# Kernel optimization log

Hardware: AMD Instinct MI355X
Metric: run time of the kernel (lower is better)

## Reference

```python
import jax, jax.numpy as jnp
import numpy as np

B, M, D, H, DH = 4, 2048, 1024, 16, 64
R_ATTN, FFN_D, R_FFN = 32, 4096, 512
ROPE_THETA = 10000.0
LN_EPS = 1e-5


def layernorm(x, w, b):
    mu = jnp.mean(x, axis=-1, keepdims=True)
    var = jnp.mean(jnp.square(x - mu), axis=-1, keepdims=True)
    return (x - mu) * jax.lax.rsqrt(var + LN_EPS) * w + b


def headwise_svd(x, U, V, b):
    # x: [B,M,D]; U: [H,D,r]; V: [H,r,dh] -> [B,M,H,dh]
    xr = jnp.einsum('bmd,hdr->bmhr', x, U)
    y = jnp.einsum('bmhr,hrk->bmhk', xr, V)
    return y + b.reshape(U.shape[0], -1)


def rotate_half(x):
    x1, x2 = jnp.split(x, 2, axis=-1)
    return jnp.concatenate([-x2, x1], axis=-1)


def rope_cos_sin(m, dh, dtype):
    inv_freq = 1.0 / (ROPE_THETA ** (jnp.arange(0, dh, 2, dtype=jnp.float32) / dh))
    freqs = jnp.arange(m, dtype=jnp.float32)[:, None] * inv_freq[None, :]  # [M, dh/2]
    emb = jnp.concatenate([freqs, freqs], axis=-1)  # [M, dh]
    return jnp.cos(emb).astype(dtype), jnp.sin(emb).astype(dtype)


def setup_inputs() -> dict:
    key = jax.random.key(0)
    ks = jax.random.split(key, 16)
    s = 0.02
    def n(k, shape, scale=s):
        return jax.random.normal(k, shape, dtype=jnp.float32) * scale
    return dict(
        hidden_states=jax.random.normal(ks[0], (B, M, D), dtype=jnp.float32),
        attention_mask=jnp.ones((B, M), dtype=jnp.int32),
        ln1_w=jnp.ones((D,), jnp.float32), ln1_b=jnp.zeros((D,), jnp.float32),
        Uq=n(ks[1], (H, D, R_ATTN)), Vq=n(ks[2], (H, R_ATTN, DH)), bq=jnp.zeros((D,), jnp.float32),
        Uk=n(ks[3], (H, D, R_ATTN)), Vk=n(ks[4], (H, R_ATTN, DH)), bk=jnp.zeros((D,), jnp.float32),
        Uv=n(ks[5], (H, D, R_ATTN)), Vv=n(ks[6], (H, R_ATTN, DH)), bv=jnp.zeros((D,), jnp.float32),
        Wo_attn=n(ks[7], (D, D)), bo_attn=jnp.zeros((D,), jnp.float32),
        ln2_w=jnp.ones((D,), jnp.float32), ln2_b=jnp.zeros((D,), jnp.float32),
        U_wi=n(ks[8], (D, R_FFN)), V_wi=n(ks[9], (R_FFN, 2 * FFN_D)), b_wi=jnp.zeros((2 * FFN_D,), jnp.float32),
        U_wo=n(ks[10], (FFN_D, R_FFN)), V_wo=n(ks[11], (R_FFN, D)), b_wo=jnp.zeros((D,), jnp.float32),
    )


def reference(hidden_states, attention_mask, ln1_w, ln1_b,
              Uq, Vq, bq, Uk, Vk, bk, Uv, Vv, bv,
              Wo_attn, bo_attn, ln2_w, ln2_b,
              U_wi, V_wi, b_wi, U_wo, V_wo, b_wo):
    x = hidden_states
    xn = layernorm(x, ln1_w, ln1_b)

    # head-wise low-rank SVD QKV projections -> [B,H,M,dh]
    q = headwise_svd(xn, Uq, Vq, bq).transpose(0, 2, 1, 3)
    k = headwise_svd(xn, Uk, Vk, bk).transpose(0, 2, 1, 3)
    v = headwise_svd(xn, Uv, Vv, bv).transpose(0, 2, 1, 3)

    cos, sin = rope_cos_sin(x.shape[1], q.shape[-1], q.dtype)  # [M, dh], broadcasts
    q = q * cos + rotate_half(q) * sin
    k = k * cos + rotate_half(k) * sin

    scale = 1.0 / jnp.sqrt(jnp.asarray(q.shape[-1], q.dtype))
    scores = jnp.einsum('bhqd,bhkd->bhqk', q, k) * scale
    pad = (attention_mask == 0)[:, None, None, :]  # [B,1,1,M]
    scores = jnp.where(pad, jnp.finfo(scores.dtype).min, scores)
    attn = jax.nn.softmax(scores, axis=-1)
    ctx = jnp.einsum('bhqk,bhkd->bhqd', attn, v)
    ctx = ctx.transpose(0, 2, 1, 3).reshape(x.shape)  # [B,M,D]
    attn_out = jnp.einsum('bmd,ed->bme', ctx, Wo_attn) + bo_attn  # dense Wo (torch Linear)
    x = x + attn_out

    # FFN: low-rank Wi -> GEGLU(tanh) -> low-rank Wo
    xn2 = layernorm(x, ln2_w, ln2_b)
    h = (xn2 @ U_wi) @ V_wi + b_wi  # [B,M,2*FFN_D]
    h1, h2 = jnp.split(h, 2, axis=-1)
    g = jax.nn.gelu(h1, approximate=True) * h2  # GEGLU, tanh approx
    ffn_out = (g @ U_wo) @ V_wo + b_wo
    return x + ffn_out
```

## Files before the change

### kernel.cpp

```cpp
#include <hip/hip_runtime.h>
#include <cstdint>

#define DEV __device__ __forceinline__

typedef __attribute__((ext_vector_type(8))) short bf16x8;
typedef __attribute__((ext_vector_type(4))) float f32x4;
typedef __attribute__((ext_vector_type(16))) float f32x16;

#define MFMA(a,b,c) __builtin_amdgcn_mfma_f32_16x16x32_bf16((a),(b),(c),0,0,0)
#define MFMA32(a,b,c) __builtin_amdgcn_mfma_f32_32x32x16_bf16((a),(b),(c),0,0,0)

DEV unsigned short f2bf(float f) {
  union { float f; unsigned u; } v; v.f = f;
  unsigned r = v.u + 0x7fffu + ((v.u >> 16) & 1u);
  return (unsigned short)(r >> 16);
}
DEV float bf2f(unsigned short s) {
  union { unsigned u; float f; } v; v.u = ((unsigned)s) << 16; return v.f;
}
DEV float max3f(float a, float b, float c) { return fmaxf(fmaxf(a, b), c); }

DEV void gload16(const unsigned short* g, short* l) {
  __builtin_amdgcn_global_load_lds(
      (const __attribute__((address_space(1))) unsigned*)g,
      (__attribute__((address_space(3))) unsigned*)l, 16, 0, 0);
}


__global__ void k_build_ut(const float* __restrict__ Uq, const float* __restrict__ Uk,
                           const float* __restrict__ Uv, unsigned short* __restrict__ Ut) {
  __shared__ float tile[32][33];
  int s = blockIdx.y;
  int proj = s >> 4, h = s & 15;
  const float* U = (proj == 0) ? Uq : (proj == 1) ? Uk : Uv;
  const float* Us = U + (size_t)h * 1024 * 32;
  int d0 = blockIdx.x * 32;
  int tx = threadIdx.x, ty = threadIdx.y;
#pragma unroll
  for (int i = ty; i < 32; i += 8)
    tile[i][tx] = Us[(size_t)(d0 + i) * 32 + tx];
  __syncthreads();
#pragma unroll
  for (int i = ty; i < 32; i += 8)
    Ut[(size_t)(s * 32 + i) * 1024 + d0 + tx] = f2bf(tile[tx][i]);
}

__global__ void k_build_vt(const float* __restrict__ Vq, const float* __restrict__ Vk,
                           const float* __restrict__ Vv, unsigned short* __restrict__ Vt) {
  int ph = blockIdx.x;
  int proj = ph >> 4, h = ph & 15;
  const float* V = (proj == 0) ? Vq : (proj == 1) ? Vk : Vv;
  const float* Vs = V + (size_t)h * 2048;
  int t = threadIdx.x;
#pragma unroll
  for (int idx = t; idx < 2048; idx += 256) {
    int dh = idx >> 5, r = idx & 31;
    Vt[(size_t)ph * 2048 + idx] = f2bf(Vs[r * 64 + dh]);
  }
}

__global__ void k_f2bf(const float* __restrict__ in, unsigned short* __restrict__ out, int n) {
  int i = blockIdx.x * 256 + threadIdx.x;
  if (i < n) out[i] = f2bf(in[i]);
}

__global__ void k_transpose_bf16(const float* __restrict__ in, unsigned short* __restrict__ out,
                                 int R, int C) {
  __shared__ float tile[32][33];
  int c0 = blockIdx.x * 32, r0 = blockIdx.y * 32;
  int tx = threadIdx.x, ty = threadIdx.y;
#pragma unroll
  for (int i = ty; i < 32; i += 8)
    tile[i][tx] = in[(size_t)(r0 + i) * C + c0 + tx];
  __syncthreads();
#pragma unroll
  for (int i = ty; i < 32; i += 8)
    out[(size_t)(c0 + i) * R + r0 + tx] = f2bf(tile[tx][i]);
}

__global__ __launch_bounds__(256) void k_layernorm(const float* __restrict__ x,
                                                   const float* __restrict__ w,
                                                   const float* __restrict__ b,
                                                   unsigned short* __restrict__ out) {
  int lane = threadIdx.x & 63, wid = threadIdx.x >> 6;
  size_t row = (size_t)blockIdx.x * 4 + wid;
  const float4* xr = (const float4*)(x + row * 1024);
  float4 v[4];
  float s = 0.f, s2 = 0.f;
#pragma unroll
  for (int t = 0; t < 4; ++t) {
    v[t] = xr[lane + t * 64];
    s += v[t].x + v[t].y + v[t].z + v[t].w;
    s2 += v[t].x * v[t].x + v[t].y * v[t].y + v[t].z * v[t].z + v[t].w * v[t].w;
  }
#pragma unroll
  for (int o = 1; o < 64; o <<= 1) { s += __shfl_xor(s, o); s2 += __shfl_xor(s2, o); }
  float mean = s * (1.f / 1024.f);
  float var = s2 * (1.f / 1024.f) - mean * mean;
  float inv = rsqrtf(var + 1e-5f);
  unsigned long long* op = (unsigned long long*)(out + row * 1024);
#pragma unroll
  for (int t = 0; t < 4; ++t) {
    float4 wv = ((const float4*)w)[lane + t * 64];
    float4 bv = ((const float4*)b)[lane + t * 64];
    union { unsigned short u[4]; unsigned long long ll; } o;
    o.u[0] = f2bf((v[t].x - mean) * inv * wv.x + bv.x);
    o.u[1] = f2bf((v[t].y - mean) * inv * wv.y + bv.y);
    o.u[2] = f2bf((v[t].z - mean) * inv * wv.z + bv.z);
    o.u[3] = f2bf((v[t].w - mean) * inv * wv.w + bv.w);
    op[lane + t * 64] = o.ll;
  }
}

template <int EPI>
__global__ __launch_bounds__(256, 4) void k_gemm(const unsigned short* __restrict__ A,
                                                 const unsigned short* __restrict__ Bt,
                                                 const float* __restrict__ bias,
                                                 const float* __restrict__ resid,
                                                 void* __restrict__ outp, int N, int K) {
  __shared__ short Al[128 * 32];
  __shared__ short Bl[128 * 32];
  int tid = threadIdx.x, lane = tid & 63, wid = tid >> 6;
  int wr = wid >> 1, wc = wid & 1;
  size_t row0 = (size_t)blockIdx.y * 128;
  int col0 = blockIdx.x * 128;
  int arow = lane >> 2, acol = (lane & 3) << 3;
  const unsigned short* Ag = A + (row0 + wid * 32 + arow) * K + acol;
  const unsigned short* Bg = Bt + ((size_t)(col0 + wid * 32 + arow)) * K + acol;
  short* Ald = Al + wid * 1024;
  short* Bld = Bl + wid * 1024;
  f32x4 acc[4][4] = {};
  int fr = lane & 15, fk = (lane >> 4) << 3;
  for (int k0 = 0; k0 < K; k0 += 32) {
    __syncthreads();
    gload16(Ag + k0, Ald);
    gload16(Ag + (size_t)16 * K + k0, Ald + 512);
    gload16(Bg + k0, Bld);
    gload16(Bg + (size_t)16 * K + k0, Bld + 512);
    __syncthreads();
    bf16x8 af[4], bfr[4];
#pragma unroll
    for (int i = 0; i < 4; ++i) {
      af[i] = *(const bf16x8*)&Al[(wr * 64 + i * 16 + fr) * 32 + fk];
      bfr[i] = *(const bf16x8*)&Bl[(wc * 64 + i * 16 + fr) * 32 + fk];
    }
#pragma unroll
    for (int i = 0; i < 4; ++i)
#pragma unroll
      for (int j = 0; j < 4; ++j) acc[i][j] = MFMA(af[i], bfr[j], acc[i][j]);
  }
  int cr = (lane >> 4) << 2, cc = lane & 15;
#pragma unroll
  for (int j = 0; j < 4; ++j) {
    int col = col0 + wc * 64 + j * 16 + cc;
    float bb = (EPI >= 1) ? bias[col] : 0.f;
#pragma unroll
    for (int i = 0; i < 4; ++i) {
#pragma unroll
      for (int r = 0; r < 4; ++r) {
        size_t row = row0 + wr * 64 + i * 16 + cr + r;
        float v = acc[i][j][r] + bb;
        if (EPI == 2)
          ((float*)outp)[row * N + col] = v + resid[row * N + col];
        else
          ((unsigned short*)outp)[row * N + col] = f2bf(v);
      }
    }
  }
}

__global__ __launch_bounds__(256, 4) void k_gemm64(const unsigned short* __restrict__ A,
                                                   const unsigned short* __restrict__ Bt,
                                                   unsigned short* __restrict__ out,
                                                   int N, int K) {
  __shared__ short Al[128 * 32];
  __shared__ short Bl[64 * 32];
  int tid = threadIdx.x, lane = tid & 63, wid = tid >> 6;
  size_t row0 = (size_t)blockIdx.y * 128;
  int col0 = blockIdx.x * 64;
  int arow = lane >> 2, acol = (lane & 3) << 3;
  const unsigned short* Ag = A + (row0 + wid * 32 + arow) * K + acol;
  const unsigned short* Bg = Bt + ((size_t)(col0 + wid * 16 + arow)) * K + acol;
  short* Ald = Al + wid * 1024;
  short* Bld = Bl + wid * 512;
  f32x4 acc[2][4] = {};
  int fr = lane & 15, fk = (lane >> 4) << 3;
  for (int k0 = 0; k0 < K; k0 += 32) {
    __syncthreads();
    gload16(Ag + k0, Ald);
    gload16(Ag + (size_t)16 * K + k0, Ald + 512);
    gload16(Bg + k0, Bld);
    __syncthreads();
    bf16x8 af[2], bfr[4];
#pragma unroll
    for (int i = 0; i < 2; ++i)
      af[i] = *(const bf16x8*)&Al[(wid * 32 + i * 16 + fr) * 32 + fk];
#pragma unroll
    for (int j = 0; j < 4; ++j)
      bfr[j] = *(const bf16x8*)&Bl[(j * 16 + fr) * 32 + fk];
#pragma unroll
    for (int i = 0; i < 2; ++i)
#pragma unroll
      for (int j = 0; j < 4; ++j) acc[i][j] = MFMA(af[i], bfr[j], acc[i][j]);
  }
  int cr = (lane >> 4) << 2, cc = lane & 15;
#pragma unroll
  for (int j = 0; j < 4; ++j) {
    int col = col0 + j * 16 + cc;
#pragma unroll
    for (int i = 0; i < 2; ++i) {
#pragma unroll
      for (int r = 0; r < 4; ++r) {
        size_t row = row0 + wid * 32 + i * 16 + cr + r;
        out[row * N + col] = f2bf(acc[i][j][r]);
      }
    }
  }
}

__global__ __launch_bounds__(256, 2) void k_qkv(const unsigned short* __restrict__ A,
                                                const unsigned short* __restrict__ Ut,
                                                const unsigned short* __restrict__ Vt,
                                                const float* __restrict__ bq,
                                                const float* __restrict__ bk,
                                                const float* __restrict__ bv,
                                                unsigned short* __restrict__ qkv,
                                                unsigned short* __restrict__ vT) {
  __shared__ short Al[128 * 32];
  __shared__ short Bl[128 * 32];
  __shared__ short Xr[4][64 * 72];
  const int K = 1024, N3 = 3072;
  int tid = threadIdx.x, lane = tid & 63, wid = tid >> 6;
  int wr = wid >> 1, wc = wid & 1;
  size_t row0 = (size_t)blockIdx.y * 128;
  int col0 = blockIdx.x * 128;
  int arow = lane >> 2, acol = (lane & 3) << 3;
  const unsigned short* Ag = A + (row0 + wid * 32 + arow) * K + acol;
  const unsigned short* Bg = Ut + ((size_t)(col0 + wid * 32 + arow)) * K + acol;
  short* Ald = Al + wid * 1024;
  short* Bld = Bl + wid * 1024;
  f32x4 acc[4][4] = {};
  int fr = lane & 15, fk = (lane >> 4) << 3;
  for (int k0 = 0; k0 < K; k0 += 32) {
    __syncthreads();
    gload16(Ag + k0, Ald);
    gload16(Ag + (size_t)16 * K + k0, Ald + 512);
    gload16(Bg + k0, Bld);
    gload16(Bg + (size_t)16 * K + k0, Bld + 512);
    __syncthreads();
    bf16x8 af[4], bfr[4];
#pragma unroll
    for (int i = 0; i < 4; ++i) {
      af[i] = *(const bf16x8*)&Al[(wr * 64 + i * 16 + fr) * 32 + fk];
      bfr[i] = *(const bf16x8*)&Bl[(wc * 64 + i * 16 + fr) * 32 + fk];
    }
#pragma unroll
    for (int i = 0; i < 4; ++i)
#pragma unroll
      for (int j = 0; j < 4; ++j) acc[i][j] = MFMA(af[i], bfr[j], acc[i][j]);
  }
  int cr = (lane >> 4) << 2, cc = lane & 15;
  short* xw = &Xr[wid][0];
#pragma unroll
  for (int j = 0; j < 4; ++j)
#pragma unroll
    for (int i = 0; i < 4; ++i)
#pragma unroll
      for (int r = 0; r < 4; ++r)
        xw[(i * 16 + cr + r) * 72 + j * 16 + cc] = (short)f2bf(acc[i][j][r]);
  int phbase = blockIdx.x * 4 + wc * 2;
  const f32x4 zero4 = {0.f, 0.f, 0.f, 0.f};
#pragma unroll
  for (int h2 = 0; h2 < 2; ++h2) {
    int ph = phbase + h2;
    int proj = ph >> 4, hh = ph & 15;
    bf16x8 af2[4], bf2[4];
#pragma unroll
    for (int i2 = 0; i2 < 4; ++i2)
      af2[i2] = *(const bf16x8*)&xw[(i2 * 16 + fr) * 72 + h2 * 32 + fk];
#pragma unroll
    for (int j2 = 0; j2 < 4; ++j2)
      bf2[j2] = *(const bf16x8*)(Vt + ((size_t)ph * 64 + j2 * 16 + fr) * 32 + fk);
    f32x4 a2[4][4];
#pragma unroll
    for (int i2 = 0; i2 < 4; ++i2)
#pragma unroll
      for (int j2 = 0; j2 < 4; ++j2) a2[i2][j2] = MFMA(af2[i2], bf2[j2], zero4);
    const float* bp = (proj == 0) ? bq : (proj == 1) ? bk : bv;
    if (proj == 2) {
      int bq_ = (int)(row0 >> 11);
      int tok0 = (int)(row0 & 2047) + wr * 64;
      unsigned short* vtb = vT + ((size_t)(bq_ * 16 + hh) * 64) * 2048;
#pragma unroll
      for (int j2 = 0; j2 < 4; ++j2) {
        int dh = j2 * 16 + cc;
        float bb = bp[hh * 64 + dh];
        unsigned short* vrow = vtb + (size_t)dh * 2048;
#pragma unroll
        for (int i2 = 0; i2 < 4; ++i2) {
          union { unsigned short u[4]; unsigned long long ll; } o;
#pragma unroll
          for (int r = 0; r < 4; ++r) o.u[r] = f2bf(a2[i2][j2][r] + bb);
          *(unsigned long long*)(vrow + tok0 + i2 * 16 + cr) = o.ll;
        }
      }
    } else {
      int obase = proj * 1024 + hh * 64;
      float sc = (proj == 0) ? 0.18033688011112042f : 1.f;
#pragma unroll
      for (int j2 = 0; j2 < 2; ++j2) {
        int irot = j2 * 16 + cc;
        float freq = __expf((float)irot * -0.28782313662425575f);
        float bb1 = bp[hh * 64 + irot];
        float bb2 = bp[hh * 64 + irot + 32];
#pragma unroll
        for (int i2 = 0; i2 < 4; ++i2)
#pragma unroll
          for (int r = 0; r < 4; ++r) {
            size_t row = row0 + wr * 64 + i2 * 16 + cr + r;
            int m = (int)(row & 2047);
            float x1v = a2[i2][j2][r] + bb1;
            float x2v = a2[i2][j2 + 2][r] + bb2;
            float sn, csn;
            __sincosf((float)m * freq, &sn, &csn);
            qkv[row * N3 + obase + irot] = f2bf((x1v * csn - x2v * sn) * sc);
            qkv[row * N3 + obase + irot + 32] = f2bf((x2v * csn + x1v * sn) * sc);
          }
      }
    }
  }
}

__global__ __launch_bounds__(256, 2) void k_gemm_geglu(const unsigned short* __restrict__ A,
                                                       const unsigned short* __restrict__ Bt,
                                                       const float* __restrict__ bias,
                                                       unsigned short* __restrict__ out) {
  __shared__ short Al[128 * 32];
  __shared__ short B1l[128 * 32];
  __shared__ short B2l[128 * 32];
  const int K = 512;
  int tid = threadIdx.x, lane = tid & 63, wid = tid >> 6;
  int wr = wid >> 1, wc = wid & 1;
  size_t row0 = (size_t)blockIdx.y * 128;
  int col0 = blockIdx.x * 128;
  int arow = lane >> 2, acol = (lane & 3) << 3;
  const unsigned short* Ag = A + (row0 + wid * 32 + arow) * K + acol;
  const unsigned short* B1g = Bt + ((size_t)(col0 + wid * 32 + arow)) * K + acol;
  const unsigned short* B2g = Bt + ((size_t)(col0 + 4096 + wid * 32 + arow)) * K + acol;
  short* Ald = Al + wid * 1024;
  short* B1d = B1l + wid * 1024;
  short* B2d = B2l + wid * 1024;
  f32x4 acc1[4][4] = {}, acc2[4][4] = {};
  int fr = lane & 15, fk = (lane >> 4) << 3;
  for (int k0 = 0; k0 < K; k0 += 32) {
    __syncthreads();
    gload16(Ag + k0, Ald);
    gload16(Ag + (size_t)16 * K + k0, Ald + 512);
    gload16(B1g + k0, B1d);
    gload16(B1g + (size_t)16 * K + k0, B1d + 512);
    gload16(B2g + k0, B2d);
    gload16(B2g + (size_t)16 * K + k0, B2d + 512);
    __syncthreads();
    bf16x8 af[4], b1f[4], b2f[4];
#pragma unroll
    for (int i = 0; i < 4; ++i) {
      af[i] = *(const bf16x8*)&Al[(wr * 64 + i * 16 + fr) * 32 + fk];
      b1f[i] = *(const bf16x8*)&B1l[(wc * 64 + i * 16 + fr) * 32 + fk];
      b2f[i] = *(const bf16x8*)&B2l[(wc * 64 + i * 16 + fr) * 32 + fk];
    }
#pragma unroll
    for (int i = 0; i < 4; ++i)
#pragma unroll
      for (int j = 0; j < 4; ++j) {
        acc1[i][j] = MFMA(af[i], b1f[j], acc1[i][j]);
        acc2[i][j] = MFMA(af[i], b2f[j], acc2[i][j]);
      }
  }
  int cr = (lane >> 4) << 2, cc = lane & 15;
#pragma unroll
  for (int j = 0; j < 4; ++j) {
    int col = col0 + wc * 64 + j * 16 + cc;
    float bb1 = bias[col], bb2 = bias[col + 4096];
#pragma unroll
    for (int i = 0; i < 4; ++i) {
#pragma unroll
      for (int r = 0; r < 4; ++r) {
        size_t row = row0 + wr * 64 + i * 16 + cr + r;
        float h1 = acc1[i][j][r] + bb1;
        float h2 = acc2[i][j][r] + bb2;
        float u = 0.7978845608028654f * (h1 + 0.044715f * h1 * h1 * h1);
        float e = __expf(2.f * u);
        float th = 1.f - 2.f / (e + 1.f);
        float gv = 0.5f * h1 * (1.f + th) * h2;
        out[row * 4096 + col] = f2bf(gv);
      }
    }
  }
}

#define KIX(r, c) ((r) * 64 + ((c) ^ (((r) & 7) << 3)))

__global__ __launch_bounds__(256, 4) void k_attn(const unsigned short* __restrict__ qkv,
                                                 const unsigned short* __restrict__ vT,
                                                 const int* __restrict__ mask,
                                                 unsigned short* __restrict__ ctx) {
  __shared__ short Kl[64 * 64];
  __shared__ short Vl[64 * 64];
  __shared__ short Ol[4][32 * 64];
  __shared__ float mpen[64];
  __shared__ int mflag;
  int bh = blockIdx.y, b = bh >> 4, h = bh & 15;
  int q0 = blockIdx.x << 7;
  int tid = threadIdx.x, lane = tid & 63, wid = tid >> 6;
  int qi = lane & 31, hi = lane >> 5;
  const unsigned short* qrow =
      qkv + ((size_t)(b * 2048 + q0 + wid * 32 + qi)) * 3072 + h * 64 + hi * 8;
  bf16x8 qa[4];
#pragma unroll
  for (int c = 0; c < 4; ++c) qa[c] = *(const bf16x8*)(qrow + c * 16);
  float m_r = -1e30f, l_r = 0.f;
  f32x16 oacc0 = {}, oacc1 = {};
  int srw = lane >> 3;
  int schx = ((lane & 7) ^ srw) << 3;
  int rb = wid * 16;
  const unsigned short* kgb =
      qkv + ((size_t)(b * 2048 + rb + srw)) * 3072 + 1024 + h * 64 + schx;
  const unsigned short* vgb = vT + ((size_t)(bh * 64 + rb + srw)) * 2048 + schx;
  short* kld = Kl + rb * 64;
  short* vld = Vl + rb * 64;
  const int* mbase = mask + b * 2048;
  const f32x16 zero16 = {};
  int mv = (tid < 64) ? mbase[tid] : 1;
  for (int k0 = 0; k0 < 2048; k0 += 64) {
    __syncthreads();
    gload16(kgb + (size_t)k0 * 3072, kld);
    gload16(kgb + (size_t)(k0 + 8) * 3072, kld + 512);
    gload16(vgb + k0, vld);
    gload16(vgb + (size_t)8 * 2048 + k0, vld + 512);
    if (wid == 0) {
      mpen[lane] = (mv == 0) ? -1e30f : 0.f;
      unsigned long long bal = __ballot(mv == 0);
      if (lane == 0) mflag = (bal != 0ull) ? 1 : 0;
    }
    if (k0 + 64 < 2048) mv = (tid < 64) ? mbase[k0 + 64 + tid] : 1;
    __syncthreads();
#pragma unroll
    for (int kt = 0; kt < 2; ++kt) {
      f32x16 s = zero16;
      __builtin_amdgcn_s_setprio(1);
#pragma unroll
      for (int c = 0; c < 4; ++c) {
        bf16x8 kf = *(const bf16x8*)&Kl[KIX(kt * 32 + qi, c * 16 + hi * 8)];
        s = MFMA32(kf, qa[c], s);
      }
      __builtin_amdgcn_s_setprio(0);
      if (mflag) {
        const f32x4* mp4 = (const f32x4*)mpen;
#pragma unroll
        for (int t = 0; t < 4; ++t) {
          f32x4 pen = mp4[kt * 8 + t * 2 + hi];
#pragma unroll
          for (int r = 0; r < 4; ++r) s[t * 4 + r] += pen[r];
        }
      }
      float t0 = max3f(s[0], s[1], s[2]);
      float t1 = max3f(s[3], s[4], s[5]);
      float t2 = max3f(s[6], s[7], s[8]);
      float t3 = max3f(s[9], s[10], s[11]);
      float t4 = max3f(s[12], s[13], s[14]);
      float t5 = fmaxf(t0, s[15]);
      float pmax = max3f(max3f(t5, t1, t2), t3, t4);
      pmax = fmaxf(pmax, __shfl_xor(pmax, 32));
      if (!__all(pmax - m_r <= 8.f)) {
        float mn = fmaxf(m_r, pmax);
        float fac = exp2f(m_r - mn);
        m_r = mn;
        l_r *= fac;
#pragma unroll
        for (int r = 0; r < 16; ++r) { oacc0[r] *= fac; oacc1[r] *= fac; }
      }
#pragma unroll
      for (int r = 0; r < 16; ++r) s[r] = exp2f(s[r] - m_r);
      float su0 = (s[0] + s[1]) + (s[2] + s[3]);
      float su1 = (s[4] + s[5]) + (s[6] + s[7]);
      float su2 = (s[8] + s[9]) + (s[10] + s[11]);
      float su3 = (s[12] + s[13]) + (s[14] + s[15]);
      l_r += (su0 + su1) + (su2 + su3);
      unsigned pk[8];
#pragma unroll
      for (int w = 0; w < 8; ++w)
        asm("v_cvt_pk_bf16_f32 %0, %1, %2" : "=v"(pk[w]) : "v"(s[2 * w]), "v"(s[2 * w + 1]));
      unsigned a0 = pk[0], b0 = pk[2];
      unsigned a1 = pk[1], b1 = pk[3];
      unsigned a2 = pk[4], b2 = pk[6];
      unsigned a3 = pk[5], b3 = pk[7];
      asm("v_permlane32_swap_b32 %0, %1" : "+v"(a0), "+v"(b0));
      asm("v_permlane32_swap_b32 %0, %1" : "+v"(a1), "+v"(b1));
      asm("v_permlane32_swap_b32 %0, %1" : "+v"(a2), "+v"(b2));
      asm("v_permlane32_swap_b32 %0, %1" : "+v"(a3), "+v"(b3));
      union { unsigned u[4]; bf16x8 v; } pb0, pb1;
      pb0.u[0] = a0; pb0.u[1] = a1; pb0.u[2] = b0; pb0.u[3] = b1;
      pb1.u[0] = a2; pb1.u[1] = a3; pb1.u[2] = b2; pb1.u[3] = b3;
      __builtin_amdgcn_s_setprio(1);
      {
        bf16x8 vf00 = *(const bf16x8*)&Vl[KIX(qi, kt * 32 + hi * 8)];
        bf16x8 vf01 = *(const bf16x8*)&Vl[KIX(qi, kt * 32 + 16 + hi * 8)];
        oacc0 = MFMA32(vf00, pb0.v, oacc0);
        oacc0 = MFMA32(vf01, pb1.v, oacc0);
        bf16x8 vf10 = *(const bf16x8*)&Vl[KIX(32 + qi, kt * 32 + hi * 8)];
        bf16x8 vf11 = *(const bf16x8*)&Vl[KIX(32 + qi, kt * 32 + 16 + hi * 8)];
        oacc1 = MFMA32(vf10, pb0.v, oacc1);
        oacc1 = MFMA32(vf11, pb1.v, oacc1);
      }
      __builtin_amdgcn_s_setprio(0);
    }
  }
  l_r += __shfl_xor(l_r, 32);
  float invl = 1.f / l_r;
  short* ob = &Ol[wid][0];
  int xsw = (qi & 7) << 3;
#pragma unroll
  for (int t = 0; t < 4; ++t) {
    int d = t * 8 + 4 * hi;
    float a0 = oacc0[4 * t] * invl, a1 = oacc0[4 * t + 1] * invl;
    float a2 = oacc0[4 * t + 2] * invl, a3 = oacc0[4 * t + 3] * invl;
    unsigned w0, w1;
    asm("v_cvt_pk_bf16_f32 %0, %1, %2" : "=v"(w0) : "v"(a0), "v"(a1));
    asm("v_cvt_pk_bf16_f32 %0, %1, %2" : "=v"(w1) : "v"(a2), "v"(a3));
    *(unsigned long long*)&ob[qi * 64 + (d ^ xsw)] =
        ((unsigned long long)w1 << 32) | (unsigned long long)w0;
    float c0 = oacc1[4 * t] * invl, c1 = oacc1[4 * t + 1] * invl;
    float c2 = oacc1[4 * t + 2] * invl, c3 = oacc1[4 * t + 3] * invl;
    unsigned w2, w3;
    asm("v_cvt_pk_bf16_f32 %0, %1, %2" : "=v"(w2) : "v"(c0), "v"(c1));
    asm("v_cvt_pk_bf16_f32 %0, %1, %2" : "=v"(w3) : "v"(c2), "v"(c3));
    *(unsigned long long*)&ob[qi * 64 + ((d + 32) ^ xsw)] =
        ((unsigned long long)w3 << 32) | (unsigned long long)w2;
  }
  __syncthreads();
#pragma unroll
  for (int p = 0; p < 2; ++p) {
    int q = p * 16 + (lane >> 2);
    int qx = (q & 7) << 3;
    unsigned short* dst =
        ctx + ((size_t)(b * 2048 + q0 + wid * 32 + q)) * 1024 + h * 64;
#pragma unroll
    for (int j = 0; j < 2; ++j) {
      int c = (lane & 3) * 8 + j * 32;
      bf16x8 vv = *(const bf16x8*)&ob[q * 64 + (c ^ qx)];
      __builtin_nontemporal_store(vv, (bf16x8*)(dst + c));
    }
  }
}

extern "C" void kernel_launch(void* const* d_in, const int* in_sizes, int n_in, void* d_out,
                              int out_size, void* d_ws, size_t ws_size, hipStream_t stream) {
  const float* x = (const float*)d_in[0];
  const int* amask = (const int*)d_in[1];
  const float* ln1w = (const float*)d_in[2];
  const float* ln1b = (const float*)d_in[3];
  const float* Uq = (const float*)d_in[4];
  const float* Vq = (const float*)d_in[5];
  const float* bq = (const float*)d_in[6];
  const float* Uk = (const float*)d_in[7];
  const float* Vk = (const float*)d_in[8];
  const float* bk = (const float*)d_in[9];
  const float* Uv = (const float*)d_in[10];
  const float* Vv = (const float*)d_in[11];
  const float* bv = (const float*)d_in[12];
  const float* Wo = (const float*)d_in[13];
  const float* bo = (const float*)d_in[14];
  const float* ln2w = (const float*)d_in[15];
  const float* ln2b = (const float*)d_in[16];
  const float* Uwi = (const float*)d_in[17];
  const float* Vwi = (const float*)d_in[18];
  const float* bwi = (const float*)d_in[19];
  const float* Uwo = (const float*)d_in[20];
  const float* Vwo = (const float*)d_in[21];
  const float* bwo = (const float*)d_in[22];

  char* ws = (char*)d_ws;
  size_t off = 0;
  auto alloc = [&](size_t bytes) {
    void* p = ws + off;
    off += (bytes + 255) & ~(size_t)255;
    return p;
  };
  unsigned short* xn = (unsigned short*)alloc((size_t)8192 * 1024 * 2);
  unsigned short* Ut = (unsigned short*)alloc((size_t)1536 * 1024 * 2);
  unsigned short* Vt = (unsigned short*)alloc((size_t)48 * 2048 * 2);
  unsigned short* Wob = (unsigned short*)alloc((size_t)1024 * 1024 * 2);
  unsigned short* Uwit = (unsigned short*)alloc((size_t)512 * 1024 * 2);
  unsigned short* Vwit = (unsigned short*)alloc((size_t)8192 * 512 * 2);
  unsigned short* Uwot = (unsigned short*)alloc((size_t)512 * 4096 * 2);
  unsigned short* Vwot = (unsigned short*)alloc((size_t)1024 * 512 * 2);
  unsigned short* qkv = (unsigned short*)alloc((size_t)8192 * 3072 * 2);
  unsigned short* ctx = (unsigned short*)alloc((size_t)8192 * 1024 * 2);
  float* x1 = (float*)alloc((size_t)8192 * 1024 * 4);
  unsigned short* hr = (unsigned short*)alloc((size_t)8192 * 512 * 2);
  unsigned short* gr = (unsigned short*)alloc((size_t)8192 * 512 * 2);
  unsigned short* g = qkv;
  unsigned short* xn2 = xn;
  unsigned short* vT = (unsigned short*)x1;
  if (off > ws_size) return;
  (void)in_sizes; (void)n_in; (void)out_size;

  dim3 tb(32, 8);
  k_build_ut<<<dim3(32, 48), tb, 0, stream>>>(Uq, Uk, Uv, Ut);
  k_build_vt<<<48, 256, 0, stream>>>(Vq, Vk, Vv, Vt);
  k_f2bf<<<4096, 256, 0, stream>>>(Wo, Wob, 1024 * 1024);
  k_transpose_bf16<<<dim3(512 / 32, 1024 / 32), tb, 0, stream>>>(Uwi, Uwit, 1024, 512);
  k_transpose_bf16<<<dim3(8192 / 32, 512 / 32), tb, 0, stream>>>(Vwi, Vwit, 512, 8192);
  k_transpose_bf16<<<dim3(512 / 32, 4096 / 32), tb, 0, stream>>>(Uwo, Uwot, 4096, 512);
  k_transpose_bf16<<<dim3(1024 / 32, 512 / 32), tb, 0, stream>>>(Vwo, Vwot, 512, 1024);

  k_layernorm<<<2048, 256, 0, stream>>>(x, ln1w, ln1b, xn);
  k_qkv<<<dim3(12, 64), 256, 0, stream>>>(xn, Ut, Vt, bq, bk, bv, qkv, vT);
  k_attn<<<dim3(16, 64), 256, 0, stream>>>(qkv, vT, amask, ctx);
  k_gemm<2><<<dim3(8, 64), 256, 0, stream>>>(ctx, Wob, bo, x, x1, 1024, 1024);
  k_layernorm<<<2048, 256, 0, stream>>>(x1, ln2w, ln2b, xn2);
  k_gemm64<<<dim3(8, 64), 256, 0, stream>>>(xn2, Uwit, hr, 512, 1024);
  k_gemm_geglu<<<dim3(32, 64), 256, 0, stream>>>(hr, Vwit, bwi, g);
  k_gemm64<<<dim3(8, 64), 256, 0, stream>>>(g, Uwot, gr, 512, 4096);
  k_gemm<2><<<dim3(8, 64), 256, 0, stream>>>(gr, Vwot, bwo, x1, d_out, 1024, 512);
}
```

Before: 474.1 us.

## Double-buffer K/V tiles in attention and precompute mask bits

The attention kernel now puts K and V into a two-stage shared-memory pool. The next 64-key tile is prefetched into the alternate buffer while the current one is computed, which drops one barrier per iteration. The per-tile mask penalty staging in shared memory is replaced by a ballot-built 32-bit mask computed up front, with per-element global reads only when a tile is masked. Shared memory per block grows to 32 KB, which could affect how many blocks fit per CU. Correctness depends on the top-of-loop barrier also waiting for the earlier async LDS loads to finish.

```diff
diff --git a/kernel.cpp b/kernel.cpp
--- a/kernel.cpp
+++ b/kernel.cpp
@@ -404,11 +404,7 @@
                                                  const unsigned short* __restrict__ vT,
                                                  const int* __restrict__ mask,
                                                  unsigned short* __restrict__ ctx) {
-  __shared__ short Kl[64 * 64];
-  __shared__ short Vl[64 * 64];
-  __shared__ short Ol[4][32 * 64];
-  __shared__ float mpen[64];
-  __shared__ int mflag;
+  __shared__ short pool[16384];
   int bh = blockIdx.y, b = bh >> 4, h = bh & 15;
   int q0 = blockIdx.x << 7;
   int tid = threadIdx.x, lane = tid & 63, wid = tid >> 6;
@@ -426,24 +422,35 @@
   const unsigned short* kgb =
       qkv + ((size_t)(b * 2048 + rb + srw)) * 3072 + 1024 + h * 64 + schx;
   const unsigned short* vgb = vT + ((size_t)(bh * 64 + rb + srw)) * 2048 + schx;
-  short* kld = Kl + rb * 64;
-  short* vld = Vl + rb * 64;
   const int* mbase = mask + b * 2048;
   const f32x16 zero16 = {};
-  int mv = (tid < 64) ? mbase[tid] : 1;
+  unsigned mbits = 0;
+  for (int t = 0; t < 32; ++t) {
+    int mv = mbase[t * 64 + lane];
+    if (__ballot(mv == 0) != 0ull) mbits |= (1u << t);
+  }
+  {
+    short* kb0 = pool + rb * 64;
+    short* vb0 = pool + 4096 + rb * 64;
+    gload16(kgb, kb0);
+    gload16(kgb + (size_t)8 * 3072, kb0 + 512);
+    gload16(vgb, vb0);
+    gload16(vgb + (size_t)8 * 2048, vb0 + 512);
+  }
+  int cur = 0;
   for (int k0 = 0; k0 < 2048; k0 += 64) {
     __syncthreads();
-    gload16(kgb + (size_t)k0 * 3072, kld);
-    gload16(kgb + (size_t)(k0 + 8) * 3072, kld + 512);
-    gload16(vgb + k0, vld);
-    gload16(vgb + (size_t)8 * 2048 + k0, vld + 512);
-    if (wid == 0) {
-      mpen[lane] = (mv == 0) ? -1e30f : 0.f;
-      unsigned long long bal = __ballot(mv == 0);
-      if (lane == 0) mflag = (bal != 0ull) ? 1 : 0;
-    }
-    if (k0 + 64 < 2048) mv = (tid < 64) ? mbase[k0 + 64 + tid] : 1;
-    __syncthreads();
+    if (k0 + 64 < 2048) {
+      short* kn = pool + (cur ^ 1) * 8192 + rb * 64;
+      short* vn = pool + (cur ^ 1) * 8192 + 4096 + rb * 64;
+      gload16(kgb + (size_t)(k0 + 64) * 3072, kn);
+      gload16(kgb + (size_t)(k0 + 72) * 3072, kn + 512);
+      gload16(vgb + (k0 + 64), vn);
+      gload16(vgb + (size_t)8 * 2048 + (k0 + 64), vn + 512);
+    }
+    const short* Kl = pool + cur * 8192;
+    const short* Vl = pool + cur * 8192 + 4096;
+    bool masked = (mbits >> (k0 >> 6)) & 1;
 #pragma unroll
     for (int kt = 0; kt < 2; ++kt) {
       f32x16 s = zero16;
@@ -454,13 +461,13 @@
         s = MFMA32(kf, qa[c], s);
       }
       __builtin_amdgcn_s_setprio(0);
-      if (mflag) {
-        const f32x4* mp4 = (const f32x4*)mpen;
+      if (masked) {
 #pragma unroll
         for (int t = 0; t < 4; ++t) {
-          f32x4 pen = mp4[kt * 8 + t * 2 + hi];
-#pragma unroll
-          for (int r = 0; r < 4; ++r) s[t * 4 + r] += pen[r];
+          int mi = k0 + kt * 32 + 8 * t + 4 * hi;
+#pragma unroll
+          for (int r = 0; r < 4; ++r)
+            s[t * 4 + r] += (mbase[mi + r] == 0) ? -1e30f : 0.f;
         }
       }
       float t0 = max3f(s[0], s[1], s[2]);
@@ -514,10 +521,12 @@
       }
       __builtin_amdgcn_s_setprio(0);
     }
+    cur ^= 1;
   }
   l_r += __shfl_xor(l_r, 32);
   float invl = 1.f / l_r;
-  short* ob = &Ol[wid][0];
+  __syncthreads();
+  short* ob = pool + wid * 2048;
   int xsw = (qi & 7) << 3;
 #pragma unroll
   for (int t = 0; t < 4; ++t) {
```

Result: no change. 472.1 us (-0.4%).
